# Performance work log

Measured on AMD Instinct MI355X. Metric: run time of the kernel, lower is better.

The kernel has to match this reference:

```python
import jax, jax.numpy as jnp
import numpy as np

D_MODEL = 1024
EXPANSION = 4
NUM_TILES = 4
D_FF = D_MODEL * EXPANSION


def setup_inputs() -> dict:
    key = jax.random.key(0)
    k1, k2, k3, k4, k5 = jax.random.split(key, 5)
    x = jax.random.normal(k1, (8, 2048, D_MODEL), dtype=jnp.float32)
    w_up = jax.random.normal(k2, (D_FF, D_MODEL), dtype=jnp.float32) * 0.02
    b_up = jax.random.normal(k3, (D_FF,), dtype=jnp.float32) * 0.02
    w_down = jax.random.normal(k4, (D_MODEL, D_FF), dtype=jnp.float32) * 0.02
    b_down = jax.random.normal(k5, (D_MODEL,), dtype=jnp.float32) * 0.02
    return {"x": x, "w_up": w_up, "b_up": b_up, "w_down": w_down, "b_down": b_down}


def reference(x, w_up, b_up, w_down, b_down):
    B, T, C = x.shape
    xf = x.reshape(B * T, C)  # [N, d_model]
    N = B * T

    # Emergent tile signatures: sign of per-tile row sums of up_proj weight.
    tile_up = D_FF // NUM_TILES
    signatures = jnp.sign(w_up.reshape(NUM_TILES, tile_up, C).sum(axis=1))  # [num_tiles, d_model]

    # Routing: argmax over input-signature alignment -> one-hot gate.
    scores = xf @ signatures.T                      # [N, num_tiles]
    winner = jnp.argmax(scores, axis=-1)            # [N]
    gate = jax.nn.one_hot(winner, NUM_TILES, dtype=xf.dtype)  # [N, num_tiles]

    # Tile-gated up projection (gate scales output tile blocks), then ReLU.
    hidden = xf @ w_up.T + b_up                     # [N, d_ff]
    hidden = (hidden.reshape(N, NUM_TILES, tile_up) * gate[:, :, None]).reshape(N, D_FF)
    hidden = jax.nn.relu(hidden)

    # Tile-gated down projection.
    tile_down = D_MODEL // NUM_TILES
    out = hidden @ w_down.T + b_down                # [N, d_model]
    out = (out.reshape(N, NUM_TILES, tile_down) * gate[:, :, None]).reshape(N, D_MODEL)

    return out.reshape(B, T, D_MODEL), gate.reshape(B, T, NUM_TILES)
```

## Files before the change

kernel.cpp:

```cpp
#include <hip/hip_runtime.h>
#include <stdint.h>
#include <stddef.h>

#define N_TOK 16384
#define DM    1024
#define DFF   4096
#define NT    4
#define TU    1024
#define TD    256

typedef __attribute__((ext_vector_type(8))) short  short8;
typedef __attribute__((ext_vector_type(4))) short  short4v;
typedef __attribute__((ext_vector_type(4))) float  floatx4;

__device__ inline unsigned short f2bf(float f){
  union { float f; uint32_t u; } v; v.f = f;
  uint32_t u = v.u + 0x7FFFu + ((v.u >> 16) & 1u);
  return (unsigned short)(u >> 16);
}

__device__ __forceinline__ void gll16(const void* g, void* l){
  __builtin_amdgcn_global_load_lds(
      (const __attribute__((address_space(1))) unsigned int*)g,
      (__attribute__((address_space(3))) unsigned int*)l,
      16, 0, 0);
}

__global__ void k_prep(const float* __restrict__ w_up,
                       const float* __restrict__ w_down,
                       float* __restrict__ partial,
                       unsigned short* __restrict__ wupb,
                       unsigned short* __restrict__ wdownb){
  const int tid = threadIdx.x;
  if (blockIdx.x >= 256){
    const size_t i = ((size_t)(blockIdx.x - 256) * 256 + tid) * 8;
    floatx4 v0 = *(const floatx4*)(w_down + i);
    floatx4 v1 = *(const floatx4*)(w_down + i + 4);
    short8 p;
    p[0]=(short)f2bf(v0[0]); p[1]=(short)f2bf(v0[1]); p[2]=(short)f2bf(v0[2]); p[3]=(short)f2bf(v0[3]);
    p[4]=(short)f2bf(v1[0]); p[5]=(short)f2bf(v1[1]); p[6]=(short)f2bf(v1[2]); p[7]=(short)f2bf(v1[3]);
    *(short8*)(wdownb + i) = p;
    return;
  }
  const int b = blockIdx.x;
  const int tile = b >> 6, chunk = b & 63;
  const int c0 = tid * 4;
  const int row0 = tile*TU + chunk*16;
  float s0=0.f, s1=0.f, s2=0.f, s3=0.f;
  const float* base = w_up + (size_t)row0 * DM + c0;
  #pragma unroll
  for (int r = 0; r < 16; ++r){
    floatx4 v = *(const floatx4*)(base + (size_t)r * DM);
    s0 += v[0]; s1 += v[1]; s2 += v[2]; s3 += v[3];
    short4v p;
    p[0]=(short)f2bf(v[0]); p[1]=(short)f2bf(v[1]);
    p[2]=(short)f2bf(v[2]); p[3]=(short)f2bf(v[3]);
    *(short4v*)(wupb + (size_t)(row0 + r) * DM + c0) = p;
  }
  float* p = partial + ((size_t)tile*DM + c0) * 64 + chunk;
  p[0] = s0; p[64] = s1; p[128] = s2; p[192] = s3;
}

__global__ void k_sig_final(const float* __restrict__ partial,
                            float* __restrict__ sig){
  const int g = blockIdx.x * 256 + threadIdx.x;
  const float* p = partial + (size_t)g * 64;
  float s = 0.f;
  #pragma unroll
  for (int i = 0; i < 64; ++i) s += p[i];
  sig[g] = (s > 0.f) ? 1.f : ((s < 0.f) ? -1.f : 0.f);
}

__global__ __launch_bounds__(256) void k_route(
    const float* __restrict__ x, const float* __restrict__ sig,
    float* __restrict__ gate_out, int* __restrict__ winner,
    unsigned short* __restrict__ xbf){
  __shared__ float ssig[NT * DM];
  const int tid = threadIdx.x;
  for (int i = tid; i < NT*DM; i += 256) ssig[i] = sig[i];
  __syncthreads();
  const int wv = tid >> 6, lane = tid & 63;

  floatx4 sg[4][4];
  #pragma unroll
  for (int j = 0; j < 4; ++j){
    const int c = j*256 + lane*4;
    #pragma unroll
    for (int tt = 0; tt < 4; ++tt)
      sg[j][tt] = *(const floatx4*)(ssig + tt*DM + c);
  }

  #pragma unroll
  for (int t = 0; t < 4; ++t){
    const int n = blockIdx.x * 16 + wv * 4 + t;
    const float* xr = x + (size_t)n * DM;
    unsigned short* xb = xbf + (size_t)n * 2048 + 1024;
    double a0=0.0, a1=0.0, a2=0.0, a3=0.0;
    #pragma unroll
    for (int j = 0; j < 4; ++j){
      const int c = j*256 + lane*4;
      floatx4 v = *(const floatx4*)(xr + c);
      short4v p;
      p[0]=(short)f2bf(v[0]); p[1]=(short)f2bf(v[1]);
      p[2]=(short)f2bf(v[2]); p[3]=(short)f2bf(v[3]);
      *(short4v*)(xb + c) = p;
      #pragma unroll
      for (int u = 0; u < 4; ++u){
        double xv = (double)v[u];
        a0 += xv * (double)sg[j][0][u];
        a1 += xv * (double)sg[j][1][u];
        a2 += xv * (double)sg[j][2][u];
        a3 += xv * (double)sg[j][3][u];
      }
    }
    #pragma unroll
    for (int off = 32; off > 0; off >>= 1){
      a0 += __shfl_down(a0, off, 64);
      a1 += __shfl_down(a1, off, 64);
      a2 += __shfl_down(a2, off, 64);
      a3 += __shfl_down(a3, off, 64);
    }
    if (lane == 0){
      double s[4] = {a0, a1, a2, a3};
      int w = 0;
      #pragma unroll
      for (int tt = 1; tt < 4; ++tt) if (s[tt] > s[w]) w = tt;
      floatx4 g = { w==0 ? 1.f:0.f, w==1 ? 1.f:0.f, w==2 ? 1.f:0.f, w==3 ? 1.f:0.f };
      *(floatx4*)(gate_out + (size_t)n * 4) = g;
      winner[n] = w;
    }
  }
}

__global__ void k_hist(const int* __restrict__ winner,
                       int* __restrict__ blk_cnt){
  __shared__ int wcnt[4][NT];
  const int tid = threadIdx.x, wv = tid >> 6, lane = tid & 63;
  const int w = winner[blockIdx.x * 256 + tid];
  #pragma unroll
  for (int t = 0; t < NT; ++t){
    unsigned long long m = __ballot(w == t);
    if (lane == 0) wcnt[wv][t] = __popcll(m);
  }
  __syncthreads();
  if (tid < NT){
    int s = wcnt[0][tid] + wcnt[1][tid] + wcnt[2][tid] + wcnt[3][tid];
    blk_cnt[blockIdx.x * NT + tid] = s;
  }
}

__global__ void k_scan(const int* __restrict__ blk_cnt,
                       int* __restrict__ meta, int* __restrict__ blk_base){
  __shared__ int s[256];
  const int tid = threadIdx.x;
  s[tid] = blk_cnt[tid];
  __syncthreads();
  if (tid == 0){
    int tot[NT] = {0,0,0,0};
    for (int b = 0; b < 64; ++b)
      for (int t = 0; t < NT; ++t) tot[t] += s[b*NT + t];
    int off = 0, base[NT];
    for (int t = 0; t < NT; ++t){ meta[t] = tot[t]; meta[4+t] = off; base[t] = off; off += tot[t]; }
    for (int b = 0; b < 64; ++b)
      for (int t = 0; t < NT; ++t){ int c = s[b*NT + t]; s[b*NT + t] = base[t]; base[t] += c; }
  }
  __syncthreads();
  blk_base[tid] = s[tid];
}

__global__ void k_scatter(const int* __restrict__ winner,
                          const int* __restrict__ blk_base,
                          int* __restrict__ idx){
  __shared__ int wcnt[4][NT];
  const int tid = threadIdx.x, wv = tid >> 6, lane = tid & 63;
  const int n = blockIdx.x * 256 + tid;
  const int w = winner[n];
  unsigned long long mymask = 0;
  #pragma unroll
  for (int t = 0; t < NT; ++t){
    unsigned long long m = __ballot(w == t);
    if (lane == 0) wcnt[wv][t] = __popcll(m);
    if (t == w) mymask = m;
  }
  __syncthreads();
  const unsigned long long below = (lane == 0) ? 0ull : (~0ull >> (64 - lane));
  int pos = blk_base[blockIdx.x * NT + w] + __popcll(mymask & below);
  for (int v = 0; v < wv; ++v) pos += wcnt[v][w];
  idx[pos] = n;
}

__global__ __launch_bounds__(256, 2) void k_gemm1(
    const unsigned short* __restrict__ xbf,
    const unsigned short* __restrict__ wupb,
    const float* __restrict__ b_up, const int* __restrict__ meta,
    const int* __restrict__ idx, unsigned short* __restrict__ hid){
  const int lin  = blockIdx.x + 128*(blockIdx.y + 8*blockIdx.z);
  const int nb   = (lin >> 3) & 7;
  const int g    = ((lin >> 6) << 3) | (lin & 7);
  const int tile = g >> 7;
  const int p0   = (g & 127) * 128;

  const int cnt  = meta[tile];
  if (p0 >= cnt) return;
  const int off  = meta[4 + tile];

  __shared__ unsigned short smem[16384];
  unsigned short* As0 = smem;
  unsigned short* As1 = smem + 4096;
  unsigned short* Bs0 = smem + 8192;
  unsigned short* Bs1 = smem + 12288;
  __shared__ int nrow[128];

  const int tid = threadIdx.x;
  if (tid < 128){
    int p = p0 + tid;
    nrow[tid] = idx[off + (p < cnt ? p : cnt - 1)];
  }
  __syncthreads();

  const int wv = tid >> 6, lane = tid & 63;
  const int wm = (wv >> 1) * 64, wn = (wv & 1) * 64;
  const int l16 = lane & 15, quad = lane >> 4;

  const int rsub = lane >> 2;
  const int kus  = (lane & 3) * 8;

  const int ra = wv*32 + rsub;
  const unsigned short* aptr0 = xbf + (size_t)nrow[ra]      * 2048 + 1024 + kus;
  const unsigned short* aptr1 = xbf + (size_t)nrow[ra + 16] * 2048 + 1024 + kus;
  const unsigned short* bptr0 = wupb + (size_t)(tile*TU + nb*128 + wv*32 + rsub) * DM + kus;
  const unsigned short* bptr1 = bptr0 + 16 * DM;

  unsigned short* a0d0 = As0 + (wv*32) * 32;  unsigned short* a0d1 = a0d0 + 16*32;
  unsigned short* a1d0 = As1 + (wv*32) * 32;  unsigned short* a1d1 = a1d0 + 16*32;
  unsigned short* b0d0 = Bs0 + (wv*32) * 32;  unsigned short* b0d1 = b0d0 + 16*32;
  unsigned short* b1d0 = Bs1 + (wv*32) * 32;  unsigned short* b1d1 = b1d0 + 16*32;

  floatx4 acc[4][4];
  #pragma unroll
  for (int i = 0; i < 4; ++i)
    #pragma unroll
    for (int j = 0; j < 4; ++j) acc[i][j] = (floatx4){0.f,0.f,0.f,0.f};

  for (int k0 = 0; k0 < DM; k0 += 64){
    gll16(aptr0 + k0,      a0d0);
    gll16(aptr1 + k0,      a0d1);
    gll16(aptr0 + k0 + 32, a1d0);
    gll16(aptr1 + k0 + 32, a1d1);
    gll16(bptr0 + k0,      b0d0);
    gll16(bptr1 + k0,      b0d1);
    gll16(bptr0 + k0 + 32, b1d0);
    gll16(bptr1 + k0 + 32, b1d1);
    __syncthreads();
    {
      short8 af[4], bfr[4];
      #pragma unroll
      for (int i = 0; i < 4; ++i) af[i]  = *(const short8*)(As0 + (wm + i*16 + l16)*32 + quad*8);
      #pragma unroll
      for (int j = 0; j < 4; ++j) bfr[j] = *(const short8*)(Bs0 + (wn + j*16 + l16)*32 + quad*8);
      #pragma unroll
      for (int i = 0; i < 4; ++i)
        #pragma unroll
        for (int j = 0; j < 4; ++j)
          acc[i][j] = __builtin_amdgcn_mfma_f32_16x16x32_bf16(af[i], bfr[j], acc[i][j], 0, 0, 0);
    }
    {
      short8 af[4], bfr[4];
      #pragma unroll
      for (int i = 0; i < 4; ++i) af[i]  = *(const short8*)(As1 + (wm + i*16 + l16)*32 + quad*8);
      #pragma unroll
      for (int j = 0; j < 4; ++j) bfr[j] = *(const short8*)(Bs1 + (wn + j*16 + l16)*32 + quad*8);
      #pragma unroll
      for (int i = 0; i < 4; ++i)
        #pragma unroll
        for (int j = 0; j < 4; ++j)
          acc[i][j] = __builtin_amdgcn_mfma_f32_16x16x32_bf16(af[i], bfr[j], acc[i][j], 0, 0, 0);
    }
    __syncthreads();
  }

  const int gcol0 = nb*128;
  #pragma unroll
  for (int half = 0; half < 2; ++half){
    if ((wv >> 1) == half){
      #pragma unroll
      for (int i = 0; i < 4; ++i){
        #pragma unroll
        for (int j = 0; j < 4; ++j){
          const int col = wn + j*16 + l16;
          const float bias = b_up[tile*TU + gcol0 + col];
          #pragma unroll
          for (int r = 0; r < 4; ++r){
            const int lrow = i*16 + quad*4 + r;
            float v = acc[i][j][r] + bias;
            smem[lrow*136 + col] = f2bf(v > 0.f ? v : 0.f);
          }
        }
      }
    }
    __syncthreads();
    #pragma unroll
    for (int c = tid; c < 1024; c += 256){
      const int lrow = c >> 4, k8 = (c & 15) * 8;
      const int m = half*64 + lrow;
      if (p0 + m < cnt){
        short8 vv = *(const short8*)(smem + lrow*136 + k8);
        *(short8*)(hid + (size_t)nrow[m]*2048 + gcol0 + k8) = vv;
      }
    }
    __syncthreads();
  }
}

__global__ __launch_bounds__(256, 2) void k_gemm2(
    const unsigned short* __restrict__ hid,
    const unsigned short* __restrict__ wdownb,
    const float* __restrict__ b_down, const int* __restrict__ meta,
    const int* __restrict__ idx, float* __restrict__ out){
  const int tile = blockIdx.z;
  const int cnt  = meta[tile];
  const int p0   = blockIdx.x * 32;
  if (p0 >= cnt) return;
  const int off  = meta[4 + tile];

  __shared__ unsigned short smem[18432];
  unsigned short* As0 = smem;
  unsigned short* As1 = smem + 1024;
  unsigned short* Bs0 = smem + 2048;
  unsigned short* Bs1 = smem + 10240;
  float* epi = (float*)smem;
  __shared__ int nrow[32];

  const int tid = threadIdx.x;
  if (tid < 32){
    int p = p0 + tid;
    nrow[tid] = idx[off + (p < cnt ? p : cnt - 1)];
  }
  __syncthreads();

  const int wv = tid >> 6, lane = tid & 63;
  const int wn = wv * 64;
  const int l16 = lane & 15, quad = lane >> 4;

  const int rsub = lane >> 2;
  const int kus  = (lane & 3) * 8;

  const int arow = (wv & 1)*16 + rsub;
  const unsigned short* aptr = hid + (size_t)nrow[arow] * 2048 + kus;
  const int aoff = (wv >> 1) * 32;
  unsigned short* asd = (wv < 2 ? As0 : As1) + ((wv & 1)*16) * 32;
  const unsigned short* bptr = wdownb + (size_t)(tile*TD + wv*64 + rsub) * DFF + tile*TU + kus;
  unsigned short* bsd0 = Bs0 + (wv*64) * 32;
  unsigned short* bsd1 = Bs1 + (wv*64) * 32;

  floatx4 acc[2][4];
  #pragma unroll
  for (int i = 0; i < 2; ++i)
    #pragma unroll
    for (int j = 0; j < 4; ++j) acc[i][j] = (floatx4){0.f,0.f,0.f,0.f};

  for (int k0 = 0; k0 < TU; k0 += 64){
    gll16(aptr + k0 + aoff, asd);
    gll16(bptr + k0,               bsd0);
    gll16(bptr + k0 + 16*DFF,      bsd0 + 16*32);
    gll16(bptr + k0 + 32*DFF,      bsd0 + 32*32);
    gll16(bptr + k0 + 48*DFF,      bsd0 + 48*32);
    gll16(bptr + k0 + 32,          bsd1);
    gll16(bptr + k0 + 32 + 16*DFF, bsd1 + 16*32);
    gll16(bptr + k0 + 32 + 32*DFF, bsd1 + 32*32);
    gll16(bptr + k0 + 32 + 48*DFF, bsd1 + 48*32);
    __syncthreads();
    {
      short8 af[2], bfr[4];
      #pragma unroll
      for (int i = 0; i < 2; ++i) af[i]  = *(const short8*)(As0 + (i*16 + l16)*32 + quad*8);
      #pragma unroll
      for (int j = 0; j < 4; ++j) bfr[j] = *(const short8*)(Bs0 + (wn + j*16 + l16)*32 + quad*8);
      #pragma unroll
      for (int i = 0; i < 2; ++i)
        #pragma unroll
        for (int j = 0; j < 4; ++j)
          acc[i][j] = __builtin_amdgcn_mfma_f32_16x16x32_bf16(af[i], bfr[j], acc[i][j], 0, 0, 0);
    }
    {
      short8 af[2], bfr[4];
      #pragma unroll
      for (int i = 0; i < 2; ++i) af[i]  = *(const short8*)(As1 + (i*16 + l16)*32 + quad*8);
      #pragma unroll
      for (int j = 0; j < 4; ++j) bfr[j] = *(const short8*)(Bs1 + (wn + j*16 + l16)*32 + quad*8);
      #pragma unroll
      for (int i = 0; i < 2; ++i)
        #pragma unroll
        for (int j = 0; j < 4; ++j)
          acc[i][j] = __builtin_amdgcn_mfma_f32_16x16x32_bf16(af[i], bfr[j], acc[i][j], 0, 0, 0);
    }
    __syncthreads();
  }

  const floatx4 z4 = {0.f, 0.f, 0.f, 0.f};
  #pragma unroll
  for (int cb = 0; cb < 4; ++cb){
    if (cb == tile) continue;
    for (int c = tid; c < 32*64; c += 256){
      const int rowl = c >> 6, c4 = (c & 63) * 4;
      if (p0 + rowl < cnt)
        *(floatx4*)(out + (size_t)nrow[rowl]*DM + cb*256 + c4) = z4;
    }
  }

  #pragma unroll
  for (int half = 0; half < 2; ++half){
    #pragma unroll
    for (int j = 0; j < 4; ++j){
      const int col = wn + j*16 + l16;
      const float bias = b_down[tile*TD + col];
      #pragma unroll
      for (int r = 0; r < 4; ++r){
        const int lrow = quad*4 + r;
        epi[lrow*260 + col] = acc[half][j][r] + bias;
      }
    }
    __syncthreads();
    #pragma unroll
    for (int c = tid; c < 1024; c += 256){
      const int lrow = c >> 6, c4 = (c & 63) * 4;
      const int m = half*16 + lrow;
      if (p0 + m < cnt){
        floatx4 v = *(const floatx4*)(epi + lrow*260 + c4);
        *(floatx4*)(out + (size_t)nrow[m]*DM + tile*TD + c4) = v;
      }
    }
    __syncthreads();
  }
}

extern "C" void kernel_launch(void* const* d_in, const int* in_sizes, int n_in,
                              void* d_out, int out_size, void* d_ws, size_t ws_size,
                              hipStream_t stream){
  const float* x      = (const float*)d_in[0];
  const float* w_up   = (const float*)d_in[1];
  const float* b_up   = (const float*)d_in[2];
  const float* w_down = (const float*)d_in[3];
  const float* b_down = (const float*)d_in[4];

  unsigned short* wupb   = (unsigned short*)d_ws;
  unsigned short* wdownb = wupb + (size_t)DFF * DM;
  float* partial = (float*)(wdownb + (size_t)DM * DFF);
  float* sig     = partial + 262144;
  int*   ints    = (int*)(sig + 4096);
  int*   winner   = ints;
  int*   idx      = ints + 16384;
  int*   meta     = ints + 32768;
  int*   blk_cnt  = ints + 32776;
  int*   blk_base = ints + 33032;

  float*          out  = (float*)d_out;
  float*          gate = out + (size_t)N_TOK * DM;
  unsigned short* ob16 = (unsigned short*)d_out;

  k_prep      <<<dim3(2304), 256, 0, stream>>>(w_up, w_down, partial, wupb, wdownb);
  k_sig_final <<<dim3(16),   256, 0, stream>>>(partial, sig);
  k_route     <<<dim3(N_TOK/16), 256, 0, stream>>>(x, sig, gate, winner, ob16);
  k_hist      <<<dim3(64),   256, 0, stream>>>(winner, blk_cnt);
  k_scan      <<<dim3(1),    256, 0, stream>>>(blk_cnt, meta, blk_base);
  k_scatter   <<<dim3(64),   256, 0, stream>>>(winner, blk_base, idx);
  k_gemm1     <<<dim3(128, 8, NT), 256, 0, stream>>>(ob16, wupb, b_up, meta, idx, ob16);
  k_gemm2     <<<dim3(512, 1, NT), 256, 0, stream>>>(ob16, wdownb, b_down, meta, idx, out);
}
```

Measured before the change: 267.1 us.

## Fuse histogram, scan and scatter into one sort kernel; interleave tiles in GEMM grids

Replaces the three routing-sort kernels (histogram, scan, scatter) with a single one-block kernel that counts, prefix-sums and scatters token indices. This removes two launches and the global round-trips for block counts and bases. It also flattens the GEMM grids and remaps block indices so that consecutive blocks cycle across the four tiles, which should spread early-exiting blocks and uneven tile loads across CUs. In exchange, the sort now runs serially in one workgroup.

```diff
diff --git a/kernel.cpp b/kernel.cpp
--- a/kernel.cpp
+++ b/kernel.cpp
@@ -132,61 +132,63 @@
   }
 }
 
-__global__ void k_hist(const int* __restrict__ winner,
-                       int* __restrict__ blk_cnt){
-  __shared__ int wcnt[4][NT];
+__global__ __launch_bounds__(256) void k_sort(const int* __restrict__ winner,
+                                              int* __restrict__ meta,
+                                              int* __restrict__ idx){
+  __shared__ int cnt_s[64][NT];
+  __shared__ int base_s[64][NT];
   const int tid = threadIdx.x, wv = tid >> 6, lane = tid & 63;
-  const int w = winner[blockIdx.x * 256 + tid];
-  #pragma unroll
-  for (int t = 0; t < NT; ++t){
-    unsigned long long m = __ballot(w == t);
-    if (lane == 0) wcnt[wv][t] = __popcll(m);
+
+  for (int seg = wv; seg < 64; seg += 4){
+    int c0 = 0, c1 = 0, c2 = 0, c3 = 0;
+    #pragma unroll
+    for (int s = 0; s < 4; ++s){
+      const int w = winner[seg*256 + s*64 + lane];
+      unsigned long long m0 = __ballot(w == 0);
+      unsigned long long m1 = __ballot(w == 1);
+      unsigned long long m2 = __ballot(w == 2);
+      unsigned long long m3 = __ballot(w == 3);
+      if (lane == 0){
+        c0 += __popcll(m0); c1 += __popcll(m1);
+        c2 += __popcll(m2); c3 += __popcll(m3);
+      }
+    }
+    if (lane == 0){
+      cnt_s[seg][0] = c0; cnt_s[seg][1] = c1;
+      cnt_s[seg][2] = c2; cnt_s[seg][3] = c3;
+    }
   }
   __syncthreads();
-  if (tid < NT){
-    int s = wcnt[0][tid] + wcnt[1][tid] + wcnt[2][tid] + wcnt[3][tid];
-    blk_cnt[blockIdx.x * NT + tid] = s;
-  }
-}
-
-__global__ void k_scan(const int* __restrict__ blk_cnt,
-                       int* __restrict__ meta, int* __restrict__ blk_base){
-  __shared__ int s[256];
-  const int tid = threadIdx.x;
-  s[tid] = blk_cnt[tid];
-  __syncthreads();
+
   if (tid == 0){
     int tot[NT] = {0,0,0,0};
     for (int b = 0; b < 64; ++b)
-      for (int t = 0; t < NT; ++t) tot[t] += s[b*NT + t];
+      for (int t = 0; t < NT; ++t) tot[t] += cnt_s[b][t];
     int off = 0, base[NT];
     for (int t = 0; t < NT; ++t){ meta[t] = tot[t]; meta[4+t] = off; base[t] = off; off += tot[t]; }
     for (int b = 0; b < 64; ++b)
-      for (int t = 0; t < NT; ++t){ int c = s[b*NT + t]; s[b*NT + t] = base[t]; base[t] += c; }
+      for (int t = 0; t < NT; ++t){ base_s[b][t] = base[t]; base[t] += cnt_s[b][t]; }
   }
   __syncthreads();
-  blk_base[tid] = s[tid];
-}
-
-__global__ void k_scatter(const int* __restrict__ winner,
-                          const int* __restrict__ blk_base,
-                          int* __restrict__ idx){
-  __shared__ int wcnt[4][NT];
-  const int tid = threadIdx.x, wv = tid >> 6, lane = tid & 63;
-  const int n = blockIdx.x * 256 + tid;
-  const int w = winner[n];
-  unsigned long long mymask = 0;
-  #pragma unroll
-  for (int t = 0; t < NT; ++t){
-    unsigned long long m = __ballot(w == t);
-    if (lane == 0) wcnt[wv][t] = __popcll(m);
-    if (t == w) mymask = m;
-  }
-  __syncthreads();
-  const unsigned long long below = (lane == 0) ? 0ull : (~0ull >> (64 - lane));
-  int pos = blk_base[blockIdx.x * NT + w] + __popcll(mymask & below);
-  for (int v = 0; v < wv; ++v) pos += wcnt[v][w];
-  idx[pos] = n;
+
+  for (int seg = wv; seg < 64; seg += 4){
+    int r0 = 0, r1 = 0, r2 = 0, r3 = 0;
+    #pragma unroll
+    for (int s = 0; s < 4; ++s){
+      const int n = seg*256 + s*64 + lane;
+      const int w = winner[n];
+      unsigned long long m0 = __ballot(w == 0);
+      unsigned long long m1 = __ballot(w == 1);
+      unsigned long long m2 = __ballot(w == 2);
+      unsigned long long m3 = __ballot(w == 3);
+      unsigned long long mymask = (w == 0) ? m0 : (w == 1) ? m1 : (w == 2) ? m2 : m3;
+      const int runw = (w == 0) ? r0 : (w == 1) ? r1 : (w == 2) ? r2 : r3;
+      const unsigned long long below = (lane == 0) ? 0ull : (~0ull >> (64 - lane));
+      idx[base_s[seg][w] + runw + __popcll(mymask & below)] = n;
+      r0 += __popcll(m0); r1 += __popcll(m1);
+      r2 += __popcll(m2); r3 += __popcll(m3);
+    }
+  }
 }
 
 __global__ __launch_bounds__(256, 2) void k_gemm1(
@@ -194,11 +196,12 @@
     const unsigned short* __restrict__ wupb,
     const float* __restrict__ b_up, const int* __restrict__ meta,
     const int* __restrict__ idx, unsigned short* __restrict__ hid){
-  const int lin  = blockIdx.x + 128*(blockIdx.y + 8*blockIdx.z);
-  const int nb   = (lin >> 3) & 7;
-  const int g    = ((lin >> 6) << 3) | (lin & 7);
-  const int tile = g >> 7;
-  const int p0   = (g & 127) * 128;
+  const int lin  = blockIdx.x;
+  const int r    = lin & 7, q = lin >> 3;
+  const int tile = r >> 1;
+  const int nb   = q & 7;
+  const int chunk = ((q >> 3) << 1) | (r & 1);
+  const int p0   = chunk * 128;
 
   const int cnt  = meta[tile];
   if (p0 >= cnt) return;
@@ -290,9 +293,9 @@
           const int col = wn + j*16 + l16;
           const float bias = b_up[tile*TU + gcol0 + col];
           #pragma unroll
-          for (int r = 0; r < 4; ++r){
-            const int lrow = i*16 + quad*4 + r;
-            float v = acc[i][j][r] + bias;
+          for (int r2 = 0; r2 < 4; ++r2){
+            const int lrow = i*16 + quad*4 + r2;
+            float v = acc[i][j][r2] + bias;
             smem[lrow*136 + col] = f2bf(v > 0.f ? v : 0.f);
           }
         }
@@ -317,9 +320,13 @@
     const unsigned short* __restrict__ wdownb,
     const float* __restrict__ b_down, const int* __restrict__ meta,
     const int* __restrict__ idx, float* __restrict__ out){
-  const int tile = blockIdx.z;
+  const int lin  = blockIdx.x;
+  const int r    = lin & 7, q = lin >> 3;
+  const int tile = r >> 1;
+  const int xx   = (q << 1) | (r & 1);
+  const int p0   = xx * 32;
+
   const int cnt  = meta[tile];
-  const int p0   = blockIdx.x * 32;
   if (p0 >= cnt) return;
   const int off  = meta[4 + tile];
 
@@ -415,9 +422,9 @@
       const int col = wn + j*16 + l16;
       const float bias = b_down[tile*TD + col];
       #pragma unroll
-      for (int r = 0; r < 4; ++r){
-        const int lrow = quad*4 + r;
-        epi[lrow*260 + col] = acc[half][j][r] + bias;
+      for (int r2 = 0; r2 < 4; ++r2){
+        const int lrow = quad*4 + r2;
+        epi[lrow*260 + col] = acc[half][j][r2] + bias;
       }
     }
     __syncthreads();
@@ -451,8 +458,6 @@
   int*   winner   = ints;
   int*   idx      = ints + 16384;
   int*   meta     = ints + 32768;
-  int*   blk_cnt  = ints + 32776;
-  int*   blk_base = ints + 33032;
 
   float*          out  = (float*)d_out;
   float*          gate = out + (size_t)N_TOK * DM;
@@ -461,9 +466,7 @@
   k_prep      <<<dim3(2304), 256, 0, stream>>>(w_up, w_down, partial, wupb, wdownb);
   k_sig_final <<<dim3(16),   256, 0, stream>>>(partial, sig);
   k_route     <<<dim3(N_TOK/16), 256, 0, stream>>>(x, sig, gate, winner, ob16);
-  k_hist      <<<dim3(64),   256, 0, stream>>>(winner, blk_cnt);
-  k_scan      <<<dim3(1),    256, 0, stream>>>(blk_cnt, meta, blk_base);
-  k_scatter   <<<dim3(64),   256, 0, stream>>>(winner, blk_base, idx);
-  k_gemm1     <<<dim3(128, 8, NT), 256, 0, stream>>>(ob16, wupb, b_up, meta, idx, ob16);
-  k_gemm2     <<<dim3(512, 1, NT), 256, 0, stream>>>(ob16, wdownb, b_down, meta, idx, out);
-}
+  k_sort      <<<dim3(1),    256, 0, stream>>>(winner, meta, idx);
+  k_gemm1     <<<dim3(4096), 256, 0, stream>>>(ob16, wupb, b_up, meta, idx, ob16);
+  k_gemm2     <<<dim3(2048), 256, 0, stream>>>(ob16, wdownb, b_down, meta, idx, out);
+}
```

Result: slower. 286.3 us (+7.2%).
